# Kernel optimization log

Hardware: AMD Instinct MI355X
Metric: run time of the kernel (lower is better)

The kernel has to match this reference:

```python
import jax, jax.numpy as jnp
import numpy as np
from jax import lax

B = 1024        # batch
K = 512         # codebook size
A = 18          # n_actions (Atari full action set)
BETA = 0.25     # commitment loss weight


def _conv(x, w, b, stride):
    # NCHW / OIHW valid conv, as nn.Conv2d with padding=0
    y = lax.conv_general_dilated(x, w, (stride, stride), 'VALID',
                                 dimension_numbers=('NCHW', 'OIHW', 'NCHW'))
    return y + b[None, :, None, None]


def _deconv(x, w, b, stride, k):
    # ConvTranspose2d(padding=0) == conv with lhs_dilation=stride, pad k-1
    y = lax.conv_general_dilated(x, w, (1, 1), [(k - 1, k - 1)] * 2,
                                 lhs_dilation=(stride, stride),
                                 dimension_numbers=('NCHW', 'OIHW', 'NCHW'))
    return y + b[None, :, None, None]


def setup_inputs() -> dict:
    key = jax.random.key(0)
    ks = jax.random.split(key, 20)
    def n(k, shape, s=0.05):
        return jax.random.normal(k, shape, jnp.float32) * s
    return {
        'x':   jax.random.uniform(ks[0], (B, 4, 84, 84), jnp.float32) * 255.0,
        'w1':  n(ks[1], (32, 4, 4, 4)),   'b1': n(ks[2], (32,)),
        'w2':  n(ks[3], (64, 32, 3, 3)),  'b2': n(ks[4], (64,)),
        'w3':  n(ks[5], (64, 64, 3, 3)),  'b3': n(ks[6], (64,)),
        'emb': n(ks[7], (K, 64), 1.0),
        'dw1': n(ks[8], (64, 64, 3, 3)),  'db1': n(ks[9], (64,)),
        'dw2': n(ks[10], (32, 64, 3, 3)), 'db2': n(ks[11], (32,)),
        'dw3': n(ks[12], (4, 32, 4, 4)),  'db3': n(ks[13], (4,)),
        'lw1': n(ks[14], (4096, 512)),    'lb1': n(ks[15], (512,)),
        'lw2': n(ks[16], (512, A)),       'lb2': n(ks[17], (A,)),
    }


def reference(x, w1, b1, w2, b2, w3, b3, emb,
              dw1, db1, dw2, db2, dw3, db3,
              lw1, lb1, lw2, lb2):
    x = x / 255.0                      # forward() scaling
    h = x / 255.0                      # encode() scales again (faithful)
    h = jax.nn.relu(_conv(h, w1, b1, 4))   # [B,32,21,21]
    h = jax.nn.relu(_conv(h, w2, b2, 2))   # [B,64,10,10]
    enc = jax.nn.relu(_conv(h, w3, b3, 1)) # [B,64,8,8]

    # --- VQ codebook lookup ---
    b_, c, hh, ww = enc.shape
    q = enc.transpose(0, 2, 3, 1).reshape(b_, hh * ww, c)      # [B,L,64]
    # squared euclidean distances to codebook (argmin identical to cdist argmin)
    d2 = (jnp.sum(q * q, -1, keepdims=True)
          - 2.0 * jnp.einsum('bld,kd->blk', q, emb)
          + jnp.sum(emb * emb, -1))                             # [B,L,K]
    idx = jnp.argmin(d2, axis=-1)                               # [B,L]
    qo = emb[idx.reshape(-1)]                                   # [B*L,64]
    qi = q.reshape(-1, c)                                       # [B*L,64]

    commitment = jnp.mean((lax.stop_gradient(qo) - qi) ** 2)
    codebook = jnp.mean((qo - lax.stop_gradient(qi)) ** 2)
    quant_loss = codebook + BETA * commitment

    st = qi + lax.stop_gradient(qo - qi)                        # straight-through
    quant = st.reshape(b_, hh, ww, c).transpose(0, 3, 1, 2)     # [B,64,8,8]

    # --- decoder ---
    d = jax.nn.relu(_deconv(quant, dw1, db1, 1, 3))  # [B,64,10,10]
    d = jax.nn.relu(_deconv(d, dw2, db2, 2, 3))      # [B,32,21,21]
    dec = jax.nn.sigmoid(_deconv(d, dw3, db3, 4, 4)) # [B,4,84,84]
    reconstruction_loss = jnp.mean((dec - x) ** 2)

    # --- Q head on detached quantized features ---
    flat = lax.stop_gradient(quant).reshape(b_, -1)             # [B,4096]
    q_values = jax.nn.relu(flat @ lw1 + lb1) @ lw2 + lb2        # [B,A]
    return (q_values, reconstruction_loss, quant_loss)
```

## Files before the change

kernel.cpp:

```cpp
#include <hip/hip_runtime.h>
#include <hip/hip_bf16.h>


#define ENC_SCALE (1.0f/65025.0f)

__global__ __launch_bounds__(256) void zero_k(float* __restrict__ hidden,
                                              float* __restrict__ accum) {
  int t = blockIdx.x * 256 + threadIdx.x;
  if (t < 524288) hidden[t] = 0.f;
  if (t < 8) accum[t] = 0.f;
}

__global__ __launch_bounds__(256) void conv1_k(
    const float* __restrict__ x, const float* __restrict__ w1,
    const float* __restrict__ b1, float* __restrict__ out) {
  int lane = threadIdx.x & 63;
  int wv = __builtin_amdgcn_readfirstlane(threadIdx.x >> 6);
  int oc0 = wv * 8;
  int p = blockIdx.x * 64 + lane;
  int b = p / 441, rem = p % 441;
  int oy = rem / 21, ox = rem % 21;
  const float* xb = x + (long)b * 28224 + (oy * 4) * 84 + ox * 4;
  const float* wp = w1 + oc0 * 64;
  float acc[8];
  #pragma unroll
  for (int c = 0; c < 8; ++c) acc[c] = b1[oc0 + c];
  #pragma unroll 1
  for (int i = 0; i < 4; ++i)
    #pragma unroll
    for (int ky = 0; ky < 4; ++ky)
      #pragma unroll
      for (int kx = 0; kx < 4; ++kx) {
        float v = xb[i * 7056 + ky * 84 + kx] * ENC_SCALE;
        int t = i * 16 + ky * 4 + kx;
        #pragma unroll
        for (int c = 0; c < 8; ++c)
          acc[c] = fmaf(v, wp[c * 64 + t], acc[c]);
      }
  float* ob = out + ((long)b * 32 + oc0) * 441 + rem;
  #pragma unroll
  for (int c = 0; c < 8; ++c) ob[c * 441] = fmaxf(acc[c], 0.f);
}

__global__ __launch_bounds__(256) void conv2_k(
    const float* __restrict__ in, const float* __restrict__ w,
    const float* __restrict__ bias, float* __restrict__ out) {
  __shared__ float in_s[32 * 441];
  int b = blockIdx.x, tid = threadIdx.x;
  const float4* src = (const float4*)(in + (long)b * 14112);
  for (int i = tid; i < 3528; i += 256) *(float4*)&in_s[i * 4] = src[i];
  __syncthreads();
  int lane = tid & 63;
  int wv = __builtin_amdgcn_readfirstlane(tid >> 6);
  int oc0 = wv * 16;
  int pxA = lane;
  int pxB = 64 + lane; if (pxB > 99) pxB = 99;
  int oyA = pxA / 10, oxA = pxA % 10;
  int oyB = pxB / 10, oxB = pxB % 10;
  float accA[16], accB[16];
  #pragma unroll
  for (int o = 0; o < 16; ++o) { float bv = bias[oc0 + o]; accA[o] = bv; accB[o] = bv; }
  #pragma unroll 2
  for (int ic = 0; ic < 32; ++ic) {
    const float* is = in_s + ic * 441;
    float a[9], bb[9];
    #pragma unroll
    for (int ky = 0; ky < 3; ++ky)
      #pragma unroll
      for (int kx = 0; kx < 3; ++kx) {
        a[ky * 3 + kx]  = is[(2 * oyA + ky) * 21 + 2 * oxA + kx];
        bb[ky * 3 + kx] = is[(2 * oyB + ky) * 21 + 2 * oxB + kx];
      }
    #pragma unroll
    for (int o = 0; o < 16; ++o) {
      const float* wp = w + (long)(oc0 + o) * 288 + ic * 9;
      #pragma unroll
      for (int t = 0; t < 9; ++t) {
        float wt = wp[t];
        accA[o] = fmaf(a[t], wt, accA[o]);
        accB[o] = fmaf(bb[t], wt, accB[o]);
      }
    }
  }
  float* ob = out + ((long)b * 64 + oc0) * 100;
  #pragma unroll
  for (int o = 0; o < 16; ++o) {
    ob[o * 100 + pxA] = fmaxf(accA[o], 0.f);
    if (lane < 36) ob[o * 100 + 64 + lane] = fmaxf(accB[o], 0.f);
  }
}

__global__ __launch_bounds__(256) void conv3_k(
    const float* __restrict__ in, const float* __restrict__ w,
    const float* __restrict__ bias, float* __restrict__ out) {
  __shared__ float in_s[6400];
  int b = blockIdx.x, tid = threadIdx.x;
  const float4* src = (const float4*)(in + (long)b * 6400);
  for (int i = tid; i < 1600; i += 256) *(float4*)&in_s[i * 4] = src[i];
  __syncthreads();
  int lane = tid & 63;
  int wv = __builtin_amdgcn_readfirstlane(tid >> 6);
  int oc0 = wv * 16;
  int oy = lane >> 3, ox = lane & 7;
  float acc[16];
  #pragma unroll
  for (int o = 0; o < 16; ++o) acc[o] = bias[oc0 + o];
  #pragma unroll 2
  for (int ic = 0; ic < 64; ++ic) {
    const float* is = in_s + ic * 100;
    float a[9];
    #pragma unroll
    for (int ky = 0; ky < 3; ++ky)
      #pragma unroll
      for (int kx = 0; kx < 3; ++kx)
        a[ky * 3 + kx] = is[(oy + ky) * 10 + ox + kx];
    #pragma unroll
    for (int o = 0; o < 16; ++o) {
      const float* wp = w + (long)(oc0 + o) * 576 + ic * 9;
      #pragma unroll
      for (int t = 0; t < 9; ++t) acc[o] = fmaf(a[t], wp[t], acc[o]);
    }
  }
  float* ob = out + ((long)b * 64 + oc0) * 64 + lane;
  #pragma unroll
  for (int o = 0; o < 16; ++o) ob[o * 64] = fmaxf(acc[o], 0.f);
}

__global__ __launch_bounds__(256) void vq_k(
    const float* __restrict__ enc, const float* __restrict__ emb,
    float* __restrict__ quant, float* __restrict__ vqpart) {
  __shared__ float ee_s[512];
  __shared__ float lsum[4];
  int tid = threadIdx.x;
  for (int k = tid; k < 512; k += 256) {
    const float* ep = emb + k * 64;
    float s = 0.f;
    #pragma unroll
    for (int d = 0; d < 64; ++d) s = fmaf(ep[d], ep[d], s);
    ee_s[k] = s;
  }
  __syncthreads();
  int w = tid >> 6, lane = tid & 63;
  int b = blockIdx.x * 4 + w;
  const float* qb = enc + ((long)b << 12) + lane;
  float q[64];
  #pragma unroll
  for (int d = 0; d < 64; ++d) q[d] = qb[d << 6];
  float qq = 0.f;
  #pragma unroll
  for (int d = 0; d < 64; ++d) qq = fmaf(q[d], q[d], qq);
  float best = 1e30f; int bk = 0;
  #pragma unroll 4
  for (int k = 0; k < 512; ++k) {
    const float* ep = emb + (k << 6);
    float dot = 0.f;
    #pragma unroll
    for (int d = 0; d < 64; ++d) dot = fmaf(q[d], ep[d], dot);
    float sc = fmaf(-2.f, dot, ee_s[k]);
    if (sc < best) { best = sc; bk = k; }
  }
  float* qo = quant + ((long)b << 12) + lane;
  const float* eb = emb + (bk << 6);
  #pragma unroll 8
  for (int d = 0; d < 64; ++d) qo[d << 6] = eb[d];
  float ls = qq + best;
  #pragma unroll
  for (int off = 32; off; off >>= 1) ls += __shfl_down(ls, off);
  if (lane == 0) lsum[w] = ls;
  __syncthreads();
  if (tid == 0) vqpart[blockIdx.x] = lsum[0] + lsum[1] + lsum[2] + lsum[3];
}

__global__ __launch_bounds__(256) void dec1_k(
    const float* __restrict__ in, const float* __restrict__ w,
    const float* __restrict__ bias, float* __restrict__ out) {
  __shared__ float in_s[64 * 144];
  int b = blockIdx.x, tid = threadIdx.x;
  for (int i = tid; i < 9216; i += 256) in_s[i] = 0.f;
  __syncthreads();
  const float* src = in + (long)b * 4096;
  for (int i = tid; i < 4096; i += 256) {
    int ic = i >> 6, p = i & 63;
    in_s[ic * 144 + (2 + (p >> 3)) * 12 + 2 + (p & 7)] = src[i];
  }
  __syncthreads();
  int lane = tid & 63;
  int wv = __builtin_amdgcn_readfirstlane(tid >> 6);
  int oc0 = wv * 16;
  int pxA = lane;
  int pxB = 64 + lane; if (pxB > 99) pxB = 99;
  int oyA = pxA / 10, oxA = pxA % 10;
  int oyB = pxB / 10, oxB = pxB % 10;
  float accA[16], accB[16];
  #pragma unroll
  for (int o = 0; o < 16; ++o) { float bv = bias[oc0 + o]; accA[o] = bv; accB[o] = bv; }
  #pragma unroll 2
  for (int ic = 0; ic < 64; ++ic) {
    const float* is = in_s + ic * 144;
    float a[9], bb[9];
    #pragma unroll
    for (int ky = 0; ky < 3; ++ky)
      #pragma unroll
      for (int kx = 0; kx < 3; ++kx) {
        a[ky * 3 + kx]  = is[(oyA + ky) * 12 + oxA + kx];
        bb[ky * 3 + kx] = is[(oyB + ky) * 12 + oxB + kx];
      }
    #pragma unroll
    for (int o = 0; o < 16; ++o) {
      const float* wp = w + (long)(oc0 + o) * 576 + ic * 9;
      #pragma unroll
      for (int t = 0; t < 9; ++t) {
        float wt = wp[t];
        accA[o] = fmaf(a[t], wt, accA[o]);
        accB[o] = fmaf(bb[t], wt, accB[o]);
      }
    }
  }
  float* ob = out + ((long)b * 64 + oc0) * 100;
  #pragma unroll
  for (int o = 0; o < 16; ++o) {
    ob[o * 100 + pxA] = fmaxf(accA[o], 0.f);
    if (lane < 36) ob[o * 100 + 64 + lane] = fmaxf(accB[o], 0.f);
  }
}

__global__ __launch_bounds__(256) void dec2_k(
    const float* __restrict__ in, const float* __restrict__ w,
    const float* __restrict__ bias, float* __restrict__ out) {
  __shared__ float in_s[64 * 144];
  int b = blockIdx.x, tid = threadIdx.x;
  for (int i = tid; i < 9216; i += 256) in_s[i] = 0.f;
  __syncthreads();
  const float* src = in + (long)b * 6400;
  for (int i = tid; i < 6400; i += 256) {
    int ic = i / 100, p = i % 100;
    in_s[ic * 144 + (p / 10) * 12 + (p % 10)] = src[i];
  }
  __syncthreads();
  int lane = tid & 63;
  int wv = __builtin_amdgcn_readfirstlane(tid >> 6);
  int oc0 = wv * 8;
  float* ob = out + ((long)b * 32 + oc0) * 441;
  float bias8[8];
  #pragma unroll
  for (int o = 0; o < 8; ++o) bias8[o] = bias[oc0 + o];

  #pragma unroll 1
  for (int pp = 0; pp < 2; ++pp) {
    int idx = pp * 64 + lane; bool okl = idx < 121; int ii = okl ? idx : 0;
    int u = ii / 11, v = ii % 11;
    float acc[8];
    #pragma unroll
    for (int o = 0; o < 8; ++o) acc[o] = bias8[o];
    #pragma unroll 2
    for (int ic = 0; ic < 64; ++ic) {
      const float* is = in_s + ic * 144;
      float i00 = is[(u + 1) * 12 + v + 1];
      float i02 = is[(u + 1) * 12 + v];
      float i20 = is[u * 12 + v + 1];
      float i22 = is[u * 12 + v];
      #pragma unroll
      for (int o = 0; o < 8; ++o) {
        const float* wp = w + (long)(oc0 + o) * 576 + ic * 9;
        acc[o] = fmaf(i00, wp[0], acc[o]);
        acc[o] = fmaf(i02, wp[2], acc[o]);
        acc[o] = fmaf(i20, wp[6], acc[o]);
        acc[o] = fmaf(i22, wp[8], acc[o]);
      }
    }
    if (okl) {
      int off = (2 * u) * 21 + 2 * v;
      #pragma unroll
      for (int o = 0; o < 8; ++o) ob[o * 441 + off] = fmaxf(acc[o], 0.f);
    }
  }
  #pragma unroll 1
  for (int pp = 0; pp < 2; ++pp) {
    int idx = pp * 64 + lane; bool okl = idx < 110; int ii = okl ? idx : 0;
    int u = ii / 10, v = ii % 10;
    float acc[8];
    #pragma unroll
    for (int o = 0; o < 8; ++o) acc[o] = bias8[o];
    #pragma unroll 2
    for (int ic = 0; ic < 64; ++ic) {
      const float* is = in_s + ic * 144;
      float i0 = is[(u + 1) * 12 + v + 1];
      float i2 = is[u * 12 + v + 1];
      #pragma unroll
      for (int o = 0; o < 8; ++o) {
        const float* wp = w + (long)(oc0 + o) * 576 + ic * 9;
        acc[o] = fmaf(i0, wp[1], acc[o]);
        acc[o] = fmaf(i2, wp[7], acc[o]);
      }
    }
    if (okl) {
      int off = (2 * u) * 21 + 2 * v + 1;
      #pragma unroll
      for (int o = 0; o < 8; ++o) ob[o * 441 + off] = fmaxf(acc[o], 0.f);
    }
  }
  #pragma unroll 1
  for (int pp = 0; pp < 2; ++pp) {
    int idx = pp * 64 + lane; bool okl = idx < 110; int ii = okl ? idx : 0;
    int u = ii / 11, v = ii % 11;
    float acc[8];
    #pragma unroll
    for (int o = 0; o < 8; ++o) acc[o] = bias8[o];
    #pragma unroll 2
    for (int ic = 0; ic < 64; ++ic) {
      const float* is = in_s + ic * 144;
      float i0 = is[(u + 1) * 12 + v + 1];
      float i2 = is[(u + 1) * 12 + v];
      #pragma unroll
      for (int o = 0; o < 8; ++o) {
        const float* wp = w + (long)(oc0 + o) * 576 + ic * 9;
        acc[o] = fmaf(i0, wp[3], acc[o]);
        acc[o] = fmaf(i2, wp[5], acc[o]);
      }
    }
    if (okl) {
      int off = (2 * u + 1) * 21 + 2 * v;
      #pragma unroll
      for (int o = 0; o < 8; ++o) ob[o * 441 + off] = fmaxf(acc[o], 0.f);
    }
  }
  #pragma unroll 1
  for (int pp = 0; pp < 2; ++pp) {
    int idx = pp * 64 + lane; bool okl = idx < 100; int ii = okl ? idx : 0;
    int u = ii / 10, v = ii % 10;
    float acc[8];
    #pragma unroll
    for (int o = 0; o < 8; ++o) acc[o] = bias8[o];
    #pragma unroll 2
    for (int ic = 0; ic < 64; ++ic) {
      const float* is = in_s + ic * 144;
      float i0 = is[(u + 1) * 12 + v + 1];
      #pragma unroll
      for (int o = 0; o < 8; ++o) {
        const float* wp = w + (long)(oc0 + o) * 576 + ic * 9;
        acc[o] = fmaf(i0, wp[4], acc[o]);
      }
    }
    if (okl) {
      int off = (2 * u + 1) * 21 + 2 * v + 1;
      #pragma unroll
      for (int o = 0; o < 8; ++o) ob[o * 441 + off] = fmaxf(acc[o], 0.f);
    }
  }
}

__global__ __launch_bounds__(256) void dec3_k(
    const float* __restrict__ d2, const float* __restrict__ dw3,
    const float* __restrict__ db3, const float* __restrict__ x,
    float* __restrict__ part) {
  int t = blockIdx.x * 256 + threadIdx.x;
  int b = t / 441, r = t % 441;
  int ty = r / 21, tx = r % 21;
  const float* ib = d2 + (long)b * 14112 + ty * 21 + tx;
  float acc[4][4][4];
  #pragma unroll
  for (int c = 0; c < 4; ++c) {
    float bv = db3[c];
    #pragma unroll
    for (int ry = 0; ry < 4; ++ry)
      #pragma unroll
      for (int rx = 0; rx < 4; ++rx) acc[c][ry][rx] = bv;
  }
  #pragma unroll 4
  for (int i = 0; i < 32; ++i) {
    float v = ib[i * 441];
    #pragma unroll
    for (int c = 0; c < 4; ++c) {
      const float* wp = dw3 + (c * 32 + i) * 16;
      #pragma unroll
      for (int ky = 0; ky < 4; ++ky) {
        float4 wv = *(const float4*)(wp + ky * 4);
        int ry = 3 - ky;
        acc[c][ry][3] = fmaf(v, wv.x, acc[c][ry][3]);
        acc[c][ry][2] = fmaf(v, wv.y, acc[c][ry][2]);
        acc[c][ry][1] = fmaf(v, wv.z, acc[c][ry][1]);
        acc[c][ry][0] = fmaf(v, wv.w, acc[c][ry][0]);
      }
    }
  }
  int y0 = ty * 4, x0 = tx * 4;
  const float* xb = x + (long)b * 28224 + y0 * 84 + x0;
  float ls = 0.f;
  #pragma unroll
  for (int c = 0; c < 4; ++c)
    #pragma unroll
    for (int ry = 0; ry < 4; ++ry) {
      float4 xv = *(const float4*)(xb + c * 7056 + ry * 84);
      float xs[4] = {xv.x, xv.y, xv.z, xv.w};
      #pragma unroll
      for (int rx = 0; rx < 4; ++rx) {
        float dec = 1.f / (1.f + __expf(-acc[c][ry][rx]));
        float df = dec - xs[rx] * (1.f / 255.f);
        ls = fmaf(df, df, ls);
      }
    }
  #pragma unroll
  for (int off = 32; off; off >>= 1) ls += __shfl_down(ls, off);
  __shared__ float r4[4];
  if ((threadIdx.x & 63) == 0) r4[threadIdx.x >> 6] = ls;
  __syncthreads();
  if (threadIdx.x == 0) part[blockIdx.x] = r4[0] + r4[1] + r4[2] + r4[3];
}

__global__ __launch_bounds__(256) void reduce_k(
    const float* __restrict__ dec3part, const float* __restrict__ vqpart,
    float* __restrict__ accum) {
  int tid = threadIdx.x;
  float s0 = 0.f, s1 = 0.f;
  for (int i = tid; i < 1764; i += 256) s0 += dec3part[i];
  if (tid < 256) s1 = vqpart[tid];
  #pragma unroll
  for (int off = 32; off; off >>= 1) {
    s0 += __shfl_down(s0, off);
    s1 += __shfl_down(s1, off);
  }
  __shared__ float a0[4], a1[4];
  int lane = tid & 63, w = tid >> 6;
  if (lane == 0) { a0[w] = s0; a1[w] = s1; }
  __syncthreads();
  if (tid == 0) {
    accum[0] = a0[0] + a0[1] + a0[2] + a0[3];
    accum[1] = a1[0] + a1[1] + a1[2] + a1[3];
  }
}

__global__ __launch_bounds__(256) void fc1_k(
    const float* __restrict__ quant, const float* __restrict__ lw1,
    float* __restrict__ hidden) {
  int n = (blockIdx.x & 1) * 256 + threadIdx.x;
  int bg = (blockIdx.x >> 1) & 63;
  int ks = blockIdx.x >> 7;
  int b0 = bg * 16;
  const float* q0 = quant + (long)b0 * 4096 + ks * 1024;
  const float* w0 = lw1 + (long)ks * 1024 * 512 + n;
  float acc[16] = {};
  #pragma unroll 4
  for (int k = 0; k < 1024; ++k) {
    float wvv = w0[(long)k * 512];
    #pragma unroll
    for (int bb = 0; bb < 16; ++bb)
      acc[bb] = fmaf(q0[bb * 4096 + k], wvv, acc[bb]);
  }
  #pragma unroll
  for (int bb = 0; bb < 16; ++bb)
    atomicAdd(&hidden[(b0 + bb) * 512 + n], acc[bb]);
}

__global__ __launch_bounds__(256) void fc2_k(
    const float* __restrict__ hidden, const float* __restrict__ lb1,
    const float* __restrict__ lw2, const float* __restrict__ lb2,
    const float* __restrict__ accum, float* __restrict__ out) {
  int t = blockIdx.x * 256 + threadIdx.x;
  int b = t / 18, a = t % 18;
  const float* h = hidden + b * 512;
  float acc = lb2[a];
  #pragma unroll 4
  for (int n = 0; n < 512; ++n) {
    float hv = fmaxf(h[n] + lb1[n], 0.f);
    acc = fmaf(hv, lw2[n * 18 + a], acc);
  }
  out[t] = acc;
  if (t == 0) {
    out[18432] = accum[0] * (1.f / 28901376.f);
    out[18433] = 1.25f * accum[1] * (1.f / 4194304.f);
  }
}

extern "C" void kernel_launch(void* const* d_in, const int* in_sizes, int n_in,
                              void* d_out, int out_size, void* d_ws, size_t ws_size,
                              hipStream_t stream) {
  const float* x   = (const float*)d_in[0];
  const float* w1  = (const float*)d_in[1];
  const float* b1  = (const float*)d_in[2];
  const float* w2  = (const float*)d_in[3];
  const float* b2  = (const float*)d_in[4];
  const float* w3  = (const float*)d_in[5];
  const float* b3  = (const float*)d_in[6];
  const float* emb = (const float*)d_in[7];
  const float* dw1 = (const float*)d_in[8];
  const float* db1 = (const float*)d_in[9];
  const float* dw2 = (const float*)d_in[10];
  const float* db2 = (const float*)d_in[11];
  const float* dw3 = (const float*)d_in[12];
  const float* db3 = (const float*)d_in[13];
  const float* lw1 = (const float*)d_in[14];
  const float* lb1 = (const float*)d_in[15];
  const float* lw2 = (const float*)d_in[16];
  const float* lb2 = (const float*)d_in[17];

  float* ws = (float*)d_ws;
  float* h1     = ws;
  float* h2     = ws + 14450688;
  float* enc    = ws + 21004288;
  float* quant  = ws + 25198592;
  float* d1     = h2;
  float* d2b    = h1;
  float* hidden = ws + 29392896;
  float* accum  = ws + 29917184;
  float* d3part = ws + 29917192;
  float* vqpart = ws + 29918956;
  float* outp   = (float*)d_out;

  zero_k<<<2048, 256, 0, stream>>>(hidden, accum);
  conv1_k<<<dim3(7056, 1), 256, 0, stream>>>(x, w1, b1, h1);
  conv2_k<<<1024, 256, 0, stream>>>(h1, w2, b2, h2);
  conv3_k<<<1024, 256, 0, stream>>>(h2, w3, b3, enc);
  vq_k<<<256, 256, 0, stream>>>(enc, emb, quant, vqpart);
  dec1_k<<<1024, 256, 0, stream>>>(quant, dw1, db1, d1);
  dec2_k<<<1024, 256, 0, stream>>>(d1, dw2, db2, d2b);
  dec3_k<<<1764, 256, 0, stream>>>(d2b, dw3, db3, x, d3part);
  reduce_k<<<1, 256, 0, stream>>>(d3part, vqpart, accum);
  fc1_k<<<512, 256, 0, stream>>>(quant, lw1, hidden);
  fc2_k<<<72, 256, 0, stream>>>(hidden, lb1, lw2, lb2, accum, outp);
}
```

Measured before the change: 1.260 ms.

## Split VQ codebook search across four waves per batch element

The VQ kernel previously gave each wave one batch element and scanned all 512 codes, using only 256 blocks. It now launches one block per batch element, with each wave scanning a 128-code slice. The per-wave minima are merged through shared memory, with ties broken toward the lower index to keep argmin semantics. The codebook row copy is split across the waves, and the partial-sum buffer grows to 1024 entries, which the reduce kernel now sums in a loop. This spreads the work over four times as many blocks to improve GPU occupancy, at the cost of each block reloading the enc tile and recomputing the codebook norms.

```diff
diff --git a/kernel.cpp b/kernel.cpp
--- a/kernel.cpp
+++ b/kernel.cpp
@@ -130,8 +130,12 @@
     const float* __restrict__ enc, const float* __restrict__ emb,
     float* __restrict__ quant, float* __restrict__ vqpart) {
   __shared__ float ee_s[512];
-  __shared__ float lsum[4];
+  __shared__ float best_s[4][64];
+  __shared__ int   bk_s[4][64];
   int tid = threadIdx.x;
+  int w = __builtin_amdgcn_readfirstlane(tid >> 6);
+  int lane = tid & 63;
+  int b = blockIdx.x;
   for (int k = tid; k < 512; k += 256) {
     const float* ep = emb + k * 64;
     float s = 0.f;
@@ -139,19 +143,16 @@
     for (int d = 0; d < 64; ++d) s = fmaf(ep[d], ep[d], s);
     ee_s[k] = s;
   }
-  __syncthreads();
-  int w = tid >> 6, lane = tid & 63;
-  int b = blockIdx.x * 4 + w;
   const float* qb = enc + ((long)b << 12) + lane;
   float q[64];
   #pragma unroll
   for (int d = 0; d < 64; ++d) q[d] = qb[d << 6];
-  float qq = 0.f;
-  #pragma unroll
-  for (int d = 0; d < 64; ++d) qq = fmaf(q[d], q[d], qq);
+  __syncthreads();
   float best = 1e30f; int bk = 0;
-  #pragma unroll 4
-  for (int k = 0; k < 512; ++k) {
+  int k0 = w * 128;
+  #pragma unroll 2
+  for (int kk = 0; kk < 128; ++kk) {
+    int k = k0 + kk;
     const float* ep = emb + (k << 6);
     float dot = 0.f;
     #pragma unroll
@@ -159,16 +160,29 @@
     float sc = fmaf(-2.f, dot, ee_s[k]);
     if (sc < best) { best = sc; bk = k; }
   }
+  best_s[w][lane] = best; bk_s[w][lane] = bk;
+  __syncthreads();
+  float cb = best_s[0][lane]; int ck = bk_s[0][lane];
+  #pragma unroll
+  for (int j = 1; j < 4; ++j) {
+    float ob = best_s[j][lane]; int ok = bk_s[j][lane];
+    if (ob < cb || (ob == cb && ok < ck)) { cb = ob; ck = ok; }
+  }
   float* qo = quant + ((long)b << 12) + lane;
-  const float* eb = emb + (bk << 6);
-  #pragma unroll 8
-  for (int d = 0; d < 64; ++d) qo[d << 6] = eb[d];
-  float ls = qq + best;
-  #pragma unroll
-  for (int off = 32; off; off >>= 1) ls += __shfl_down(ls, off);
-  if (lane == 0) lsum[w] = ls;
-  __syncthreads();
-  if (tid == 0) vqpart[blockIdx.x] = lsum[0] + lsum[1] + lsum[2] + lsum[3];
+  #pragma unroll
+  for (int j = 0; j < 16; ++j) {
+    int d = w * 16 + j;
+    qo[d << 6] = emb[ck * 64 + d];
+  }
+  if (w == 0) {
+    float qq = 0.f;
+    #pragma unroll
+    for (int d = 0; d < 64; ++d) qq = fmaf(q[d], q[d], qq);
+    float ls = qq + cb;
+    #pragma unroll
+    for (int off = 32; off; off >>= 1) ls += __shfl_down(ls, off);
+    if (lane == 0) vqpart[b] = ls;
+  }
 }
 
 __global__ __launch_bounds__(256) void dec1_k(
@@ -413,7 +427,7 @@
   int tid = threadIdx.x;
   float s0 = 0.f, s1 = 0.f;
   for (int i = tid; i < 1764; i += 256) s0 += dec3part[i];
-  if (tid < 256) s1 = vqpart[tid];
+  for (int i = tid; i < 1024; i += 256) s1 += vqpart[i];
   #pragma unroll
   for (int off = 32; off; off >>= 1) {
     s0 += __shfl_down(s0, off);
@@ -510,7 +524,7 @@
   conv1_k<<<dim3(7056, 1), 256, 0, stream>>>(x, w1, b1, h1);
   conv2_k<<<1024, 256, 0, stream>>>(h1, w2, b2, h2);
   conv3_k<<<1024, 256, 0, stream>>>(h2, w3, b3, enc);
-  vq_k<<<256, 256, 0, stream>>>(enc, emb, quant, vqpart);
+  vq_k<<<1024, 256, 0, stream>>>(enc, emb, quant, vqpart);
   dec1_k<<<1024, 256, 0, stream>>>(quant, dw1, db1, d1);
   dec2_k<<<1024, 256, 0, stream>>>(d1, dw2, db2, d2b);
   dec3_k<<<1764, 256, 0, stream>>>(d2b, dw3, db3, x, d3part);
```

After: 1.107 ms. 12.2% less time.
